# Kernel tuning notes

Measured on AMD Instinct MI355X. Metric: run time of the kernel, lower is better.

## Reference

```python
import jax, jax.numpy as jnp
import numpy as np

N = 20000       # nodes
E = 320000      # edges
D_IN = 128
H = 512
OUT = 7
EPS = 1e-5


def setup_inputs() -> dict:
    key = jax.random.key(0)
    ks = jax.random.split(key, 16)
    def lin(k, fan_in, fan_out):
        bound = 1.0 / np.sqrt(fan_in)
        kw, kb = jax.random.split(k)
        W = jax.random.uniform(kw, (fan_in, fan_out), jnp.float32, -bound, bound)
        b = jax.random.uniform(kb, (fan_out,), jnp.float32, -bound, bound)
        return W, b
    x = jax.random.normal(ks[0], (N, D_IN), jnp.float32)
    edge_index = jax.random.randint(ks[1], (2, E), 0, N, dtype=jnp.int64)
    W1, b1 = lin(ks[2], D_IN, H)
    W2, b2 = lin(ks[3], H, H)
    W3, b3 = lin(ks[4], H, H)
    W4, b4 = lin(ks[5], H, H)
    ln_gamma = jnp.ones((H,), jnp.float32)
    ln_beta = jnp.zeros((H,), jnp.float32)
    W_out, b_out = lin(ks[6], H, OUT)
    return {"x": x, "edge_index": edge_index,
            "W1": W1, "b1": b1, "W2": W2, "b2": b2,
            "W3": W3, "b3": b3, "W4": W4, "b4": b4,
            "ln_gamma": ln_gamma, "ln_beta": ln_beta,
            "W_out": W_out, "b_out": b_out}


def _gcn_layer(x, W, b, src, dst, dinv):
    # transform, then symmetric-normalized gather/scatter-add (PyG GCNConv)
    h = x @ W                                    # [N, H]
    norm = dinv[src] * dinv[dst]                 # [E+N]
    msg = h[src] * norm[:, None]                 # gather + scale
    agg = jax.ops.segment_sum(msg, dst, num_segments=N)
    return agg + b


def reference(x, edge_index, W1, b1, W2, b2, W3, b3, W4, b4,
              ln_gamma, ln_beta, W_out, b_out):
    loops = jnp.arange(N, dtype=edge_index.dtype)
    src = jnp.concatenate([edge_index[0], loops])  # A + I self loops
    dst = jnp.concatenate([edge_index[1], loops])
    deg = jax.ops.segment_sum(jnp.ones_like(src, dtype=x.dtype), dst,
                              num_segments=N)
    dinv = jnp.where(deg > 0, jax.lax.rsqrt(deg), 0.0)

    def ln(h):
        mu = h.mean(-1, keepdims=True)
        var = h.var(-1, keepdims=True)
        return (h - mu) * jax.lax.rsqrt(var + EPS) * ln_gamma + ln_beta

    for W, b in ((W1, b1), (W2, b2), (W3, b3), (W4, b4)):
        x = jax.nn.relu(ln(_gcn_layer(x, W, b, src, dst, dinv)))
    g = x.mean(axis=0)           # mean pool over nodes -> [H]
    # dropout is identity in eval mode
    return g @ W_out + b_out     # [OUT]
```

## Files before the change

kernel.cpp:

```cpp
#include <hip/hip_runtime.h>

#define HID 512
#define OUTD 7
#define EPSV 1e-5f

typedef __attribute__((ext_vector_type(8))) short bf16x8;
typedef __attribute__((ext_vector_type(4))) float f32x4;
typedef __attribute__((ext_vector_type(2))) float f32x2;
typedef unsigned short ushort_t;
typedef unsigned int uint_t;
typedef unsigned char uchar_t;

__device__ __forceinline__ ushort_t f2bf(float f) {
    uint_t u = __float_as_uint(f);
    u = (u + 0x7fffu + ((u >> 16) & 1u)) >> 16;
    return (ushort_t)u;
}
__device__ __forceinline__ float bflo(uint_t u) { return __uint_as_float(u << 16); }
__device__ __forceinline__ float bfhi(uint_t u) { return __uint_as_float(u & 0xffff0000u); }

__device__ __forceinline__ void dec4(uint_t v, float* f) {
    f32x2 p0 = __builtin_amdgcn_cvt_pk_f32_fp8(v, false);
    f32x2 p1 = __builtin_amdgcn_cvt_pk_f32_fp8(v, true);
    f[0] = p0.x; f[1] = p0.y; f[2] = p1.x; f[3] = p1.y;
}
__device__ __forceinline__ uint_t enc4(float a, float b, float c, float d) {
    uint_t r = __builtin_amdgcn_cvt_pk_fp8_f32(a, b, 0, false);
    r = __builtin_amdgcn_cvt_pk_fp8_f32(c, d, r, true);
    return r;
}

__device__ __forceinline__ void gload_lds16(const ushort_t* g, ushort_t* l) {
    __builtin_amdgcn_global_load_lds(
        (const __attribute__((address_space(1))) uint_t*)g,
        (__attribute__((address_space(3))) uint_t*)l, 16, 0, 0);
}


__global__ void zero_deg(int* __restrict__ deg, int N) {
    int i = blockIdx.x * blockDim.x + threadIdx.x;
    if (i < N) deg[i] = 0;
}

__global__ void setup2(const int* __restrict__ dst, int* __restrict__ deg, int E,
                       const float* __restrict__ W0, const float* __restrict__ W1,
                       const float* __restrict__ W2, const float* __restrict__ W3,
                       ushort_t* __restrict__ T0, ushort_t* __restrict__ T1,
                       ushort_t* __restrict__ T2, ushort_t* __restrict__ T3) {
    int i = blockIdx.x * blockDim.x + threadIdx.x;
    if (i < E) { atomicAdd(&deg[dst[i]], 1); return; }
    i -= E;
    const int S0 = 128 * HID, S1 = HID * HID;
    if (i < S0) { int k = i / HID, n = i % HID; T0[(size_t)n * 128 + k] = f2bf(W0[i]); return; }
    i -= S0;
    if (i < S1) { int k = i / HID, n = i % HID; T1[(size_t)n * HID + k] = f2bf(W1[i]); return; }
    i -= S1;
    if (i < S1) { int k = i / HID, n = i % HID; T2[(size_t)n * HID + k] = f2bf(W2[i]); return; }
    i -= S1;
    if (i < S1) { int k = i / HID, n = i % HID; T3[(size_t)n * HID + k] = f2bf(W3[i]); }
}


__global__ void scan1(const int* __restrict__ deg, int* __restrict__ off,
                      int* __restrict__ partial, float* __restrict__ dinv, int N) {
    __shared__ int s[256];
    const int t = threadIdx.x;
    const int i = blockIdx.x * 256 + t;
    int d = (i < N) ? deg[i] : 0;
    if (i < N) dinv[i] = rsqrtf((float)(d + 1));
    s[t] = d;
    __syncthreads();
#pragma unroll
    for (int ofs = 1; ofs < 256; ofs <<= 1) {
        int v = (t >= ofs) ? s[t - ofs] : 0;
        __syncthreads();
        s[t] += v;
        __syncthreads();
    }
    if (i < N) off[i] = s[t] - d;
    if (t == 255) partial[blockIdx.x] = s[255];
}

__global__ void scan2(int* __restrict__ partial, int nb) {
    __shared__ int s[256];
    const int t = threadIdx.x;
    int d = (t < nb) ? partial[t] : 0;
    s[t] = d;
    __syncthreads();
#pragma unroll
    for (int ofs = 1; ofs < 256; ofs <<= 1) {
        int v = (t >= ofs) ? s[t - ofs] : 0;
        __syncthreads();
        s[t] += v;
        __syncthreads();
    }
    if (t < nb) partial[t] = s[t] - d;
}

__global__ void scan3(int* __restrict__ off, const int* __restrict__ partial,
                      int* __restrict__ cursor, int N, int E) {
    int i = blockIdx.x * blockDim.x + threadIdx.x;
    if (i < N) {
        int v = off[i] + partial[i >> 8];
        off[i] = v;
        cursor[i] = v;
    } else if (i == N) {
        off[N] = E;
    }
}


__global__ void fill_cvt(const int* __restrict__ src, const int* __restrict__ dst,
                         int* __restrict__ cursor, int* __restrict__ srcs, int E,
                         const float* __restrict__ x, const float* __restrict__ dinv,
                         ushort_t* __restrict__ xb, int pairs, float* __restrict__ gsum) {
    int i = blockIdx.x * blockDim.x + threadIdx.x;
    if (i < E) { int p = atomicAdd(&cursor[dst[i]], 1); srcs[p] = src[i]; return; }
    i -= E;
    if (i < pairs) {
        float dr = dinv[i >> 6];
        float a = x[2 * i] * dr, b = x[2 * i + 1] * dr;
        uint_t d = __builtin_amdgcn_cvt_pk_fp8_f32(a, b, 0, false);
        xb[i] = (ushort_t)(d & 0xffffu);
        return;
    }
    i -= pairs;
    if (i < HID) gsum[i] = 0.0f;
}


__global__ __launch_bounds__(256) void csr_agg_512(
        const uchar_t* __restrict__ xs, const int* __restrict__ off,
        const int* __restrict__ srcs, const float* __restrict__ dinv,
        ushort_t* __restrict__ ax, int N) {
    int gtid = blockIdx.x * 256 + threadIdx.x;
    int r = gtid >> 6, lane = gtid & 63;
    if (r >= N) return;
    const uint2* xb = (const uint2*)xs;
    float a[8];
    {
        uint2 v = xb[(size_t)r * 64 + lane];
        dec4(v.x, a); dec4(v.y, a + 4);
    }
    int e = off[r];
    const int e1 = off[r + 1];
    for (; e + 8 <= e1; e += 8) {
        int si[8]; uint2 vi[8];
#pragma unroll
        for (int j = 0; j < 8; j++) si[j] = srcs[e + j];
#pragma unroll
        for (int j = 0; j < 8; j++) vi[j] = xb[(size_t)si[j] * 64 + lane];
#pragma unroll
        for (int j = 0; j < 8; j++) {
            float f[8]; dec4(vi[j].x, f); dec4(vi[j].y, f + 4);
#pragma unroll
            for (int q = 0; q < 8; q++) a[q] += f[q];
        }
    }
    for (; e < e1; e++) {
        uint2 v = xb[(size_t)srcs[e] * 64 + lane];
        float f[8]; dec4(v.x, f); dec4(v.y, f + 4);
#pragma unroll
        for (int q = 0; q < 8; q++) a[q] += f[q];
    }
    float dr = dinv[r];
    uint4 o;
    o.x = (uint_t)f2bf(a[0] * dr) | ((uint_t)f2bf(a[1] * dr) << 16);
    o.y = (uint_t)f2bf(a[2] * dr) | ((uint_t)f2bf(a[3] * dr) << 16);
    o.z = (uint_t)f2bf(a[4] * dr) | ((uint_t)f2bf(a[5] * dr) << 16);
    o.w = (uint_t)f2bf(a[6] * dr) | ((uint_t)f2bf(a[7] * dr) << 16);
    ((uint4*)ax)[(size_t)r * 64 + lane] = o;
}

__global__ __launch_bounds__(256) void csr_agg_128(
        const uchar_t* __restrict__ xs, const int* __restrict__ off,
        const int* __restrict__ srcs, const float* __restrict__ dinv,
        ushort_t* __restrict__ ax, int N) {
    int gtid = blockIdx.x * 256 + threadIdx.x;
    int r = gtid >> 6, lane = gtid & 63;
    if (r >= N) return;
    const ushort_t* xb = (const ushort_t*)xs;
    float a0, a1;
    {
        uint_t v = xb[(size_t)r * 64 + lane];
        f32x2 p = __builtin_amdgcn_cvt_pk_f32_fp8(v, false);
        a0 = p.x; a1 = p.y;
    }
    int e = off[r];
    const int e1 = off[r + 1];
    for (; e + 8 <= e1; e += 8) {
        int si[8]; uint_t vi[8];
#pragma unroll
        for (int j = 0; j < 8; j++) si[j] = srcs[e + j];
#pragma unroll
        for (int j = 0; j < 8; j++) vi[j] = xb[(size_t)si[j] * 64 + lane];
#pragma unroll
        for (int j = 0; j < 8; j++) {
            f32x2 p = __builtin_amdgcn_cvt_pk_f32_fp8(vi[j], false);
            a0 += p.x; a1 += p.y;
        }
    }
    for (; e < e1; e++) {
        uint_t v = xb[(size_t)srcs[e] * 64 + lane];
        f32x2 p = __builtin_amdgcn_cvt_pk_f32_fp8(v, false);
        a0 += p.x; a1 += p.y;
    }
    float dr = dinv[r];
    ((uint_t*)ax)[(size_t)r * 64 + lane] =
        (uint_t)f2bf(a0 * dr) | ((uint_t)f2bf(a1 * dr) << 16);
}


__global__ __launch_bounds__(256) void gemm_mfma(
        const ushort_t* __restrict__ A, const ushort_t* __restrict__ Wt,
        const float* __restrict__ bias, ushort_t* __restrict__ C, int M, int K) {
    __shared__ __align__(16) ushort_t As[4 * 128 * 8];
    __shared__ __align__(16) ushort_t Bs[4 * 128 * 8];
    const int t = threadIdx.x;
    const int wave = t >> 6, lane = t & 63;
    const int m0 = blockIdx.y * 128, n0 = blockIdx.x * 128;
    const int wm = (wave & 1) * 64, wn = (wave >> 1) * 64;
    const int quad = lane >> 4, l16 = lane & 15;

    f32x4 acc[4][4];
#pragma unroll
    for (int i = 0; i < 4; i++)
#pragma unroll
        for (int j = 0; j < 4; j++) acc[i][j] = (f32x4){0.f, 0.f, 0.f, 0.f};

    for (int k0 = 0; k0 < K; k0 += 32) {
        const int c = wave;
#pragma unroll
        for (int h = 0; h < 2; h++) {
            int gm = m0 + 64 * h + lane;
            if (gm >= M) gm = M - 1;
            gload_lds16(A + (size_t)gm * K + k0 + c * 8, &As[(c * 128 + 64 * h) * 8]);
            gload_lds16(Wt + (size_t)(n0 + 64 * h + lane) * K + k0 + c * 8,
                        &Bs[(c * 128 + 64 * h) * 8]);
        }
        __syncthreads();
        bf16x8 af[4], bfr[4];
#pragma unroll
        for (int i = 0; i < 4; i++) {
            af[i]  = *(const bf16x8*)&As[(quad * 128 + wm + i * 16 + l16) * 8];
            bfr[i] = *(const bf16x8*)&Bs[(quad * 128 + wn + i * 16 + l16) * 8];
        }
#pragma unroll
        for (int i = 0; i < 4; i++)
#pragma unroll
            for (int jn = 0; jn < 4; jn++)
                acc[i][jn] = __builtin_amdgcn_mfma_f32_16x16x32_bf16(
                                 af[i], bfr[jn], acc[i][jn], 0, 0, 0);
        __syncthreads();
    }
#pragma unroll
    for (int i = 0; i < 4; i++) {
#pragma unroll
        for (int jn = 0; jn < 4; jn++) {
            int gn = n0 + wn + jn * 16 + l16;
            float bv = bias[gn];
#pragma unroll
            for (int rg = 0; rg < 4; rg++) {
                int gm = m0 + wm + i * 16 + quad * 4 + rg;
                if (gm < M) C[(size_t)gm * HID + gn] = f2bf(acc[i][jn][rg] + bv);
            }
        }
    }
}


template<int MODE>
__global__ void ln_relu(const ushort_t* __restrict__ h, const float* __restrict__ gamma,
                        const float* __restrict__ beta, const float* __restrict__ dinv,
                        void* __restrict__ optr, int N) {
    int gtid = blockIdx.x * blockDim.x + threadIdx.x;
    int r = gtid >> 6, lane = gtid & 63;
    if (r >= N) return;
    uint4 v = ((const uint4*)(h + (size_t)r * HID))[lane];
    float f[8] = {bflo(v.x), bfhi(v.x), bflo(v.y), bfhi(v.y),
                  bflo(v.z), bfhi(v.z), bflo(v.w), bfhi(v.w)};
    float s = 0.f, q = 0.f;
#pragma unroll
    for (int j = 0; j < 8; j++) { s += f[j]; q += f[j] * f[j]; }
#pragma unroll
    for (int ofs = 32; ofs > 0; ofs >>= 1) {
        s += __shfl_xor(s, ofs);
        q += __shfl_xor(q, ofs);
    }
    float mu  = s * (1.0f / HID);
    float var = q * (1.0f / HID) - mu * mu;
    float rs  = rsqrtf(var + EPSV);
    float dr  = (MODE == 1) ? dinv[r] : 1.0f;
    const float4* gp = (const float4*)gamma;
    const float4* bp = (const float4*)beta;
    float4 g0 = gp[2 * lane], g1 = gp[2 * lane + 1];
    float4 b0 = bp[2 * lane], b1 = bp[2 * lane + 1];
    float gg[8] = {g0.x, g0.y, g0.z, g0.w, g1.x, g1.y, g1.z, g1.w};
    float bb[8] = {b0.x, b0.y, b0.z, b0.w, b1.x, b1.y, b1.z, b1.w};
    float o[8];
#pragma unroll
    for (int j = 0; j < 8; j++)
        o[j] = fmaxf((f[j] - mu) * rs * gg[j] + bb[j], 0.f) * dr;
    if (MODE == 0) {
        uint4 ov;
        ov.x = (uint_t)f2bf(o[0]) | ((uint_t)f2bf(o[1]) << 16);
        ov.y = (uint_t)f2bf(o[2]) | ((uint_t)f2bf(o[3]) << 16);
        ov.z = (uint_t)f2bf(o[4]) | ((uint_t)f2bf(o[5]) << 16);
        ov.w = (uint_t)f2bf(o[6]) | ((uint_t)f2bf(o[7]) << 16);
        ((uint4*)optr)[(size_t)r * 64 + lane] = ov;
    } else {
        uint2 ov;
        ov.x = enc4(o[0], o[1], o[2], o[3]);
        ov.y = enc4(o[4], o[5], o[6], o[7]);
        ((uint2*)optr)[(size_t)r * 64 + lane] = ov;
    }
}


__global__ void colsum(const ushort_t* __restrict__ h, float* __restrict__ gsum, int N) {
    int t = threadIdx.x;
    float a0 = 0.f, a1 = 0.f;
    for (int r = blockIdx.x; r < N; r += gridDim.x) {
        uint_t u = ((const uint_t*)(h + (size_t)r * HID))[t];
        a0 += bflo(u);
        a1 += bfhi(u);
    }
    atomicAdd(&gsum[2 * t], a0);
    atomicAdd(&gsum[2 * t + 1], a1);
}

__global__ void out_kernel(const float* __restrict__ gsum, const float* __restrict__ Wout,
                           const float* __restrict__ bout, float* __restrict__ out, int N) {
    __shared__ float red[256];
    int t = threadIdx.x;
    float g0 = gsum[2 * t], g1 = gsum[2 * t + 1];
    float invn = 1.0f / (float)N;
    for (int o = 0; o < OUTD; o++) {
        float p = g0 * Wout[(2 * t) * OUTD + o] + g1 * Wout[(2 * t + 1) * OUTD + o];
        red[t] = p;
        __syncthreads();
        for (int sft = 128; sft > 0; sft >>= 1) {
            if (t < sft) red[t] += red[t + sft];
            __syncthreads();
        }
        if (t == 0) out[o] = red[0] * invn + bout[o];
        __syncthreads();
    }
}


extern "C" void kernel_launch(void* const* d_in, const int* in_sizes, int n_in,
                              void* d_out, int out_size, void* d_ws, size_t ws_size,
                              hipStream_t stream) {
    const float* x  = (const float*)d_in[0];
    const int*   ei = (const int*)d_in[1];
    const int N = in_sizes[0] / 128;
    const int E = in_sizes[1] / 2;
    const int* src = ei;
    const int* dst = ei + E;
    const float* Ws[4] = {(const float*)d_in[2], (const float*)d_in[4],
                          (const float*)d_in[6], (const float*)d_in[8]};
    const float* bs[4] = {(const float*)d_in[3], (const float*)d_in[5],
                          (const float*)d_in[7], (const float*)d_in[9]};
    const float* gamma = (const float*)d_in[10];
    const float* beta  = (const float*)d_in[11];
    const float* Wout  = (const float*)d_in[12];
    const float* bout  = (const float*)d_in[13];
    float* out = (float*)d_out;

    char* p = (char*)d_ws;
    ushort_t* axb = (ushort_t*)p;  p += sizeof(ushort_t) * (size_t)N * HID;
    ushort_t* hb  = (ushort_t*)p;  p += sizeof(ushort_t) * (size_t)N * HID;
    uchar_t*  ho8 = (uchar_t*)p;   p += (size_t)N * HID;
    uchar_t*  xb8 = ho8;
    ushort_t* Wt[4];
    Wt[0] = (ushort_t*)p;          p += sizeof(ushort_t) * 128 * HID;
    Wt[1] = (ushort_t*)p;          p += sizeof(ushort_t) * HID * HID;
    Wt[2] = (ushort_t*)p;          p += sizeof(ushort_t) * HID * HID;
    Wt[3] = (ushort_t*)p;          p += sizeof(ushort_t) * HID * HID;
    float* dinv = (float*)p;       p += sizeof(float) * N;
    float* gsum = (float*)p;       p += sizeof(float) * HID;
    int* deg    = (int*)p;         p += sizeof(int) * N;
    int* off    = (int*)p;         p += sizeof(int) * (N + 4);
    int* cursor = (int*)p;         p += sizeof(int) * N;
    int* partial= (int*)p;         p += sizeof(int) * 256;
    int* srcs   = (int*)p;

    const int nb = (N + 255) / 256;

    zero_deg<<<(N + 255) / 256, 256, 0, stream>>>(deg, N);
    {
        int tot = E + 128 * HID + 3 * HID * HID;
        setup2<<<(tot + 255) / 256, 256, 0, stream>>>(dst, deg, E, Ws[0], Ws[1], Ws[2], Ws[3],
                                                      Wt[0], Wt[1], Wt[2], Wt[3]);
    }
    scan1<<<nb, 256, 0, stream>>>(deg, off, partial, dinv, N);
    scan2<<<1, 256, 0, stream>>>(partial, nb);
    scan3<<<(N + 256) / 256, 256, 0, stream>>>(off, partial, cursor, N, E);
    {
        int pairs = N * 64;
        int tot = E + pairs + HID;
        fill_cvt<<<(tot + 255) / 256, 256, 0, stream>>>(src, dst, cursor, srcs, E,
                                                        x, dinv, (ushort_t*)xb8, pairs, gsum);
    }

    for (int l = 0; l < 4; l++) {
        const int K = (l == 0) ? 128 : HID;
        if (l == 0)
            csr_agg_128<<<(N * 64 + 255) / 256, 256, 0, stream>>>(xb8, off, srcs, dinv, axb, N);
        else
            csr_agg_512<<<(N * 64 + 255) / 256, 256, 0, stream>>>(ho8, off, srcs, dinv, axb, N);
        dim3 gg(HID / 128, (N + 127) / 128);
        gemm_mfma<<<gg, 256, 0, stream>>>(axb, Wt[l], bs[l], hb, N, K);
        if (l < 3)
            ln_relu<1><<<(N * 64 + 255) / 256, 256, 0, stream>>>(hb, gamma, beta, dinv, ho8, N);
        else
            ln_relu<0><<<(N * 64 + 255) / 256, 256, 0, stream>>>(hb, gamma, beta, dinv, axb, N);
    }
    colsum<<<512, 256, 0, stream>>>(axb, gsum, N);
    out_kernel<<<1, 256, 0, stream>>>(gsum, Wout, bout, out, N);
}
```

Baseline: 412.4 us.

## Store aggregated activations as fp8 and decode to bf16 inside the GEMM

The aggregation kernels now write their output in fp8 instead of bf16, which halves the intermediate write and the GEMM A-operand read. The GEMM loads fp8 A tiles into LDS, converts them to bf16 in registers before the MFMA, and steps K by 64 per iteration with a larger B tile. The two small scan kernels are merged into one by having every block redo the tiny partial scan. The final layer norm writes in place into the bf16 buffer. The cost is lower precision on the GEMM input, plus extra conversion ALU work in the GEMM inner loop.

```diff
diff --git a/kernel.cpp b/kernel.cpp
--- a/kernel.cpp
+++ b/kernel.cpp
@@ -31,6 +31,11 @@
 }
 
 __device__ __forceinline__ void gload_lds16(const ushort_t* g, ushort_t* l) {
+    __builtin_amdgcn_global_load_lds(
+        (const __attribute__((address_space(1))) uint_t*)g,
+        (__attribute__((address_space(3))) uint_t*)l, 16, 0, 0);
+}
+__device__ __forceinline__ void gload_lds16_u8(const uchar_t* g, uchar_t* l) {
     __builtin_amdgcn_global_load_lds(
         (const __attribute__((address_space(1))) uint_t*)g,
         (__attribute__((address_space(3))) uint_t*)l, 16, 0, 0);
@@ -81,8 +86,10 @@
     if (t == 255) partial[blockIdx.x] = s[255];
 }
 
-__global__ void scan2(int* __restrict__ partial, int nb) {
+__global__ void scan23(int* __restrict__ off, const int* __restrict__ partial,
+                       int* __restrict__ cursor, int N, int E, int nb) {
     __shared__ int s[256];
+    __shared__ int ex[256];
     const int t = threadIdx.x;
     int d = (t < nb) ? partial[t] : 0;
     s[t] = d;
@@ -94,14 +101,11 @@
         s[t] += v;
         __syncthreads();
     }
-    if (t < nb) partial[t] = s[t] - d;
-}
-
-__global__ void scan3(int* __restrict__ off, const int* __restrict__ partial,
-                      int* __restrict__ cursor, int N, int E) {
-    int i = blockIdx.x * blockDim.x + threadIdx.x;
+    ex[t] = s[t] - d;
+    __syncthreads();
+    int i = blockIdx.x * 256 + t;
     if (i < N) {
-        int v = off[i] + partial[i >> 8];
+        int v = off[i] + ex[i >> 8];
         off[i] = v;
         cursor[i] = v;
     } else if (i == N) {
@@ -132,7 +136,7 @@
 __global__ __launch_bounds__(256) void csr_agg_512(
         const uchar_t* __restrict__ xs, const int* __restrict__ off,
         const int* __restrict__ srcs, const float* __restrict__ dinv,
-        ushort_t* __restrict__ ax, int N) {
+        uchar_t* __restrict__ ax, int N) {
     int gtid = blockIdx.x * 256 + threadIdx.x;
     int r = gtid >> 6, lane = gtid & 63;
     if (r >= N) return;
@@ -164,18 +168,16 @@
         for (int q = 0; q < 8; q++) a[q] += f[q];
     }
     float dr = dinv[r];
-    uint4 o;
-    o.x = (uint_t)f2bf(a[0] * dr) | ((uint_t)f2bf(a[1] * dr) << 16);
-    o.y = (uint_t)f2bf(a[2] * dr) | ((uint_t)f2bf(a[3] * dr) << 16);
-    o.z = (uint_t)f2bf(a[4] * dr) | ((uint_t)f2bf(a[5] * dr) << 16);
-    o.w = (uint_t)f2bf(a[6] * dr) | ((uint_t)f2bf(a[7] * dr) << 16);
-    ((uint4*)ax)[(size_t)r * 64 + lane] = o;
+    uint2 o;
+    o.x = enc4(a[0] * dr, a[1] * dr, a[2] * dr, a[3] * dr);
+    o.y = enc4(a[4] * dr, a[5] * dr, a[6] * dr, a[7] * dr);
+    ((uint2*)ax)[(size_t)r * 64 + lane] = o;
 }
 
 __global__ __launch_bounds__(256) void csr_agg_128(
         const uchar_t* __restrict__ xs, const int* __restrict__ off,
         const int* __restrict__ srcs, const float* __restrict__ dinv,
-        ushort_t* __restrict__ ax, int N) {
+        uchar_t* __restrict__ ax, int N) {
     int gtid = blockIdx.x * 256 + threadIdx.x;
     int r = gtid >> 6, lane = gtid & 63;
     if (r >= N) return;
@@ -206,16 +208,16 @@
         a0 += p.x; a1 += p.y;
     }
     float dr = dinv[r];
-    ((uint_t*)ax)[(size_t)r * 64 + lane] =
-        (uint_t)f2bf(a0 * dr) | ((uint_t)f2bf(a1 * dr) << 16);
+    uint_t d = __builtin_amdgcn_cvt_pk_fp8_f32(a0 * dr, a1 * dr, 0, false);
+    ((ushort_t*)ax)[(size_t)r * 64 + lane] = (ushort_t)(d & 0xffffu);
 }
 
 
 __global__ __launch_bounds__(256) void gemm_mfma(
-        const ushort_t* __restrict__ A, const ushort_t* __restrict__ Wt,
+        const uchar_t* __restrict__ A, const ushort_t* __restrict__ Wt,
         const float* __restrict__ bias, ushort_t* __restrict__ C, int M, int K) {
-    __shared__ __align__(16) ushort_t As[4 * 128 * 8];
-    __shared__ __align__(16) ushort_t Bs[4 * 128 * 8];
+    __shared__ __align__(16) uchar_t  As[4 * 128 * 16];
+    __shared__ __align__(16) ushort_t Bs[8 * 128 * 8];
     const int t = threadIdx.x;
     const int wave = t >> 6, lane = t & 63;
     const int m0 = blockIdx.y * 128, n0 = blockIdx.x * 128;
@@ -228,29 +230,50 @@
 #pragma unroll
         for (int j = 0; j < 4; j++) acc[i][j] = (f32x4){0.f, 0.f, 0.f, 0.f};
 
-    for (int k0 = 0; k0 < K; k0 += 32) {
-        const int c = wave;
+    for (int k0 = 0; k0 < K; k0 += 64) {
 #pragma unroll
         for (int h = 0; h < 2; h++) {
             int gm = m0 + 64 * h + lane;
             if (gm >= M) gm = M - 1;
-            gload_lds16(A + (size_t)gm * K + k0 + c * 8, &As[(c * 128 + 64 * h) * 8]);
-            gload_lds16(Wt + (size_t)(n0 + 64 * h + lane) * K + k0 + c * 8,
-                        &Bs[(c * 128 + 64 * h) * 8]);
-        }
-        __syncthreads();
-        bf16x8 af[4], bfr[4];
-#pragma unroll
-        for (int i = 0; i < 4; i++) {
-            af[i]  = *(const bf16x8*)&As[(quad * 128 + wm + i * 16 + l16) * 8];
-            bfr[i] = *(const bf16x8*)&Bs[(quad * 128 + wn + i * 16 + l16) * 8];
-        }
-#pragma unroll
-        for (int i = 0; i < 4; i++)
+            gload_lds16_u8(A + (size_t)gm * K + k0 + wave * 16,
+                           &As[(wave * 128 + 64 * h) * 16]);
+        }
+#pragma unroll
+        for (int h = 0; h < 4; h++) {
+            int cb = wave * 2 + (h >> 1);
+            int row = (h & 1) * 64 + lane;
+            gload_lds16(Wt + (size_t)(n0 + row) * K + k0 + cb * 8,
+                        &Bs[(cb * 128 + (h & 1) * 64) * 8]);
+        }
+        __syncthreads();
+#pragma unroll
+        for (int kk = 0; kk < 2; kk++) {
+            bf16x8 af[4], bfr[4];
 #pragma unroll
             for (int jn = 0; jn < 4; jn++)
-                acc[i][jn] = __builtin_amdgcn_mfma_f32_16x16x32_bf16(
-                                 af[i], bfr[jn], acc[i][jn], 0, 0, 0);
+                bfr[jn] = *(const bf16x8*)&Bs[((kk * 4 + quad) * 128 + wn + jn * 16 + l16) * 8];
+#pragma unroll
+            for (int i = 0; i < 4; i++) {
+                uint2 v8 = *(const uint2*)&As[((kk * 2 + (quad >> 1)) * 128 + wm + i * 16 + l16) * 16
+                                              + (quad & 1) * 8];
+                f32x2 p0 = __builtin_amdgcn_cvt_pk_f32_fp8(v8.x, false);
+                f32x2 p1 = __builtin_amdgcn_cvt_pk_f32_fp8(v8.x, true);
+                f32x2 p2 = __builtin_amdgcn_cvt_pk_f32_fp8(v8.y, false);
+                f32x2 p3 = __builtin_amdgcn_cvt_pk_f32_fp8(v8.y, true);
+                union { uint_t u[4]; bf16x8 v; } pk;
+                pk.u[0] = (__float_as_uint(p0.y) & 0xffff0000u) | (__float_as_uint(p0.x) >> 16);
+                pk.u[1] = (__float_as_uint(p1.y) & 0xffff0000u) | (__float_as_uint(p1.x) >> 16);
+                pk.u[2] = (__float_as_uint(p2.y) & 0xffff0000u) | (__float_as_uint(p2.x) >> 16);
+                pk.u[3] = (__float_as_uint(p3.y) & 0xffff0000u) | (__float_as_uint(p3.x) >> 16);
+                af[i] = pk.v;
+            }
+#pragma unroll
+            for (int i = 0; i < 4; i++)
+#pragma unroll
+                for (int jn = 0; jn < 4; jn++)
+                    acc[i][jn] = __builtin_amdgcn_mfma_f32_16x16x32_bf16(
+                                     af[i], bfr[jn], acc[i][jn], 0, 0, 0);
+        }
         __syncthreads();
     }
 #pragma unroll
@@ -369,7 +392,7 @@
     float* out = (float*)d_out;
 
     char* p = (char*)d_ws;
-    ushort_t* axb = (ushort_t*)p;  p += sizeof(ushort_t) * (size_t)N * HID;
+    uchar_t*  axb = (uchar_t*)p;   p += (size_t)N * HID;
     ushort_t* hb  = (ushort_t*)p;  p += sizeof(ushort_t) * (size_t)N * HID;
     uchar_t*  ho8 = (uchar_t*)p;   p += (size_t)N * HID;
     uchar_t*  xb8 = ho8;
@@ -395,8 +418,7 @@
                                                       Wt[0], Wt[1], Wt[2], Wt[3]);
     }
     scan1<<<nb, 256, 0, stream>>>(deg, off, partial, dinv, N);
-    scan2<<<1, 256, 0, stream>>>(partial, nb);
-    scan3<<<(N + 256) / 256, 256, 0, stream>>>(off, partial, cursor, N, E);
+    scan23<<<(N + 256) / 256, 256, 0, stream>>>(off, partial, cursor, N, E, nb);
     {
         int pairs = N * 64;
         int tot = E + pairs + HID;
@@ -415,8 +437,8 @@
         if (l < 3)
             ln_relu<1><<<(N * 64 + 255) / 256, 256, 0, stream>>>(hb, gamma, beta, dinv, ho8, N);
         else
-            ln_relu<0><<<(N * 64 + 255) / 256, 256, 0, stream>>>(hb, gamma, beta, dinv, axb, N);
-    }
-    colsum<<<512, 256, 0, stream>>>(axb, gsum, N);
+            ln_relu<0><<<(N * 64 + 255) / 256, 256, 0, stream>>>(hb, gamma, beta, dinv, hb, N);
+    }
+    colsum<<<512, 256, 0, stream>>>(hb, gsum, N);
     out_kernel<<<1, 256, 0, stream>>>(gsum, Wout, bout, out, N);
 }
```

Measured after the change: 395.3 us. 4.2% less time.
